# Performance work log

Hardware: AMD Instinct MI355X
Metric: run time of the kernel (lower is better)

## Reference

```python
import jax, jax.numpy as jnp
import numpy as np

WIN_SIZE = 16
STRIDE = 8
H = W = 512
B = 8
C = 3


def gaussian_blend(win_size):
    # matches WindowOverlapProcessor._create_gaussian_weights
    sigma = win_size / 4.0
    x = jnp.arange(win_size, dtype=jnp.float32) - (win_size - 1) / 2.0
    g = jnp.exp(-(x ** 2) / (2.0 * sigma ** 2))
    g = g / g.sum()
    return g[:, None] * g[None, :]  # [ws, ws]


def setup_inputs() -> dict:
    key = jax.random.key(0)
    hw = (H - WIN_SIZE) // STRIDE + 1  # 63
    ww = (W - WIN_SIZE) // STRIDE + 1  # 63
    nw = hw * ww  # 3969
    hs = (jnp.arange(hw) * STRIDE).astype(jnp.int64 if jax.config.jax_enable_x64 else jnp.int32)
    ws_ = (jnp.arange(ww) * STRIDE).astype(hs.dtype)
    coords = jnp.stack(
        [jnp.repeat(hs, ww), jnp.tile(ws_, hw)], axis=-1
    )  # [nw, 2] regular overlapping grid
    windows = jax.random.normal(key, (B, nw, WIN_SIZE, WIN_SIZE, C), dtype=jnp.float32)
    return {
        "windows": windows,
        "window_coords": coords,
        "h_windows": hw,
        "w_windows": ww,
        "stride": STRIDE,
        "original_h": H,
        "original_w": W,
        "channels": C,
    }


def reference(windows, window_coords, h_windows, w_windows, stride,
              original_h, original_w, channels):
    Bb, nw, ws, _, Cc = windows.shape
    blend = gaussian_blend(ws)  # [ws, ws]

    # flat pixel index for every window element
    dh = jnp.arange(ws)
    dw = jnp.arange(ws)
    offs = dh[:, None] * original_w + dw[None, :]            # [ws, ws]
    base = window_coords[:, 0] * original_w + window_coords[:, 1]  # [nw]
    idx = (base[:, None, None] + offs[None]).reshape(-1)     # [nw*ws*ws]

    # weighted window values, [B, C, nw*ws*ws]
    contrib = windows * blend[None, None, :, :, None]
    contrib = contrib.transpose(0, 4, 1, 2, 3).reshape(Bb, Cc, -1)

    recon = jnp.zeros((Bb, Cc, original_h * original_w), windows.dtype)
    recon = recon.at[:, :, idx].add(contrib)

    wsum = jnp.zeros((original_h * original_w,), blend.dtype)
    wsum = wsum.at[idx].add(jnp.tile(blend.reshape(-1), nw))

    recon = recon / (wsum[None, None, :] + 1e-8)
    return recon.reshape(Bb, Cc, original_h, original_w)
```

## Files before the change

kernel.cpp:

```cpp
#include <hip/hip_runtime.h>


#define OH 512
#define OW 512
#define NB 8
#define NC 3
#define HWIN 63
#define NWIN (HWIN * HWIN)
#define PLANE (OH * OW)
#define CH_F4 96
#define NCHUNK 34
#define NF4 (NCHUNK * CH_F4)
#define NSTRIPE (NF4 / 64)
#define STRIPE_PAD 65

typedef float f4 __attribute__((ext_vector_type(4)));
typedef unsigned int u32;

__device__ __forceinline__ float gblend(int d) {
    const float x = (float)d - 7.5f;
    return __expf(-(x * x) * 0.03125f) * 0.1044284f;
}

__device__ __forceinline__ int pof(int F) { return F + (F >> 6); }

__device__ __forceinline__ void async_ld16(const f4* gsrc, f4* ldst) {
    __builtin_amdgcn_global_load_lds(
        (const __attribute__((address_space(1))) u32*)gsrc,
        (__attribute__((address_space(3))) u32*)ldst, 16, 0, 0);
}

__global__ __launch_bounds__(256, 3) void window_overlap_kernel(
    const float* __restrict__ win, float* __restrict__ out) {
    __shared__ f4 lds[NSTRIPE * STRIPE_PAD];

    const int tid = threadIdx.x;
    const int bi = blockIdx.x;
    const int t = bi & 3;
    const int q = (bi >> 2) & 63;
    const int b = bi >> 8;

    const int qL = min(q, 62);
    const int qH = max(q - 1, 0);
    const int bOff = b * NWIN;

    const f4* __restrict__ w4 = (const f4*)win;
    const int wv = tid >> 6;
    const int lane = tid & 63;
    for (int s = wv; s < NSTRIPE; s += 4) {
        const int F = s * 64 + lane;
        const int c = F / 96;
        const int e = F - c * 96;
        const int hi = (c >= 17) ? 1 : 0;
        const int k = c - hi * 17;
        const int jj = min(max(16 * t - 1 + k, 0), HWIN - 1);
        const int qr = hi ? qH : qL;
        const int gidx = (bOff + qr * HWIN + jj) * 192 + hi * CH_F4 + e;
        async_ld16(w4 + gidx, &lds[s * STRIPE_PAD]);
    }
    __syncthreads();

    const int r = tid >> 5;
    const int w4p = (tid & 31) << 2;
    const int jl = w4p >> 3;
    const int c0 = w4p & 7;
    const int jg = 16 * t + jl;
    const float fB = (jg <= HWIN - 1) ? 1.0f : 0.0f;
    const float fA = (jg >= 1) ? 1.0f : 0.0f;
    const float wT = (q <= 62) ? gblend(r) : 0.0f;
    const float wB = (q >= 1) ? gblend(r + 8) : 0.0f;

    const int s0 = (c0 >> 2) * 3;
    const int rowf = r * 12;
    const int FLoB = (jl + 1) * 96 + rowf + s0;
    const int FLoA = jl * 96 + rowf + 6 + s0;
    const int FHiB = (18 + jl) * 96 + rowf + s0;
    const int FHiA = (17 + jl) * 96 + rowf + 6 + s0;

    f4 lb[3], la[3], hb[3], ha[3];
#pragma unroll
    for (int k = 0; k < 3; ++k) {
        lb[k] = lds[pof(FLoB + k)];
        la[k] = lds[pof(FLoA + k)];
        hb[k] = lds[pof(FHiB + k)];
        ha[k] = lds[pof(FHiA + k)];
    }

    const f4 gB = c0 ? (f4){0.0712141f, 0.0859006f, 0.0973380f, 0.1036157f}
                     : (f4){0.0180058f, 0.0278880f, 0.0405766f, 0.0554615f};
    const f4 gA = c0 ? (f4){0.0554615f, 0.0405766f, 0.0278880f, 0.0180058f}
                     : (f4){0.1036157f, 0.0973380f, 0.0859006f, 0.0712141f};

    f4 o[NC];
#pragma unroll
    for (int m = 0; m < 4; ++m) {
        const float wBc = fB * gB[m];
        const float wAc = fA * gA[m];
        const float rn = __builtin_amdgcn_rcpf((wT + wB) * (wAc + wBc) + 1e-8f);
#pragma unroll
        for (int ch = 0; ch < NC; ++ch) {
            const int f = 3 * m + ch;
            const float v = wT * (wAc * la[f >> 2][f & 3] + wBc * lb[f >> 2][f & 3]) +
                            wB * (wAc * ha[f >> 2][f & 3] + wBc * hb[f >> 2][f & 3]);
            o[ch][m] = v * rn;
        }
    }

    const int p = b * (NC * PLANE) + (8 * q + r) * OW + 128 * t + w4p;
    __builtin_nontemporal_store(o[0], (f4*)&out[p]);
    __builtin_nontemporal_store(o[1], (f4*)&out[p + PLANE]);
    __builtin_nontemporal_store(o[2], (f4*)&out[p + 2 * PLANE]);
}

extern "C" void kernel_launch(void* const* d_in, const int* in_sizes, int n_in,
                              void* d_out, int out_size, void* d_ws, size_t ws_size,
                              hipStream_t stream) {
    const float* windows = (const float*)d_in[0];
    float* out = (float*)d_out;
    window_overlap_kernel<<<2048, 256, 0, stream>>>(windows, out);
}
```

Before: 159.5 us.

## Split each tile into single-wave blocks covering two output rows

Each 256-thread block handling eight output rows is replaced by four 64-thread blocks, each handling two rows. A block now loads only the window rows it needs (24 float4 per chunk, padded to 25) into a smaller LDS buffer. The padding function is dropped and block indices are swizzled. The aim is higher occupancy and less LDS per block, so memory latency is better hidden and tail effects shrink. In exchange there are four times as many blocks, and nearby window data is fetched by separate blocks with more scattered loads.

New measurement: 159.8 us. No clear change (+0.2%).

```diff
diff --git a/kernel.cpp b/kernel.cpp
--- a/kernel.cpp
+++ b/kernel.cpp
@@ -8,11 +8,6 @@
 #define HWIN 63
 #define NWIN (HWIN * HWIN)
 #define PLANE (OH * OW)
-#define CH_F4 96
-#define NCHUNK 34
-#define NF4 (NCHUNK * CH_F4)
-#define NSTRIPE (NF4 / 64)
-#define STRIPE_PAD 65
 
 typedef float f4 __attribute__((ext_vector_type(4)));
 typedef unsigned int u32;
@@ -22,68 +17,71 @@
     return __expf(-(x * x) * 0.03125f) * 0.1044284f;
 }
 
-__device__ __forceinline__ int pof(int F) { return F + (F >> 6); }
-
 __device__ __forceinline__ void async_ld16(const f4* gsrc, f4* ldst) {
     __builtin_amdgcn_global_load_lds(
         (const __attribute__((address_space(1))) u32*)gsrc,
         (__attribute__((address_space(3))) u32*)ldst, 16, 0, 0);
 }
 
-__global__ __launch_bounds__(256, 3) void window_overlap_kernel(
+__global__ __launch_bounds__(64) void window_overlap_kernel(
     const float* __restrict__ win, float* __restrict__ out) {
-    __shared__ f4 lds[NSTRIPE * STRIPE_PAD];
+    __shared__ f4 lds[896];
 
-    const int tid = threadIdx.x;
     const int bi = blockIdx.x;
-    const int t = bi & 3;
-    const int q = (bi >> 2) & 63;
-    const int b = bi >> 8;
+    const int rp = (bi >> 3) & 3;
+    const int u = (bi & 7) | ((bi >> 5) << 3);
+    const int t = u & 3;
+    const int q = (u >> 2) & 63;
+    const int b = u >> 8;
+    const int r0 = rp << 1;
 
     const int qL = min(q, 62);
     const int qH = max(q - 1, 0);
     const int bOff = b * NWIN;
+    const int lane = threadIdx.x;
 
     const f4* __restrict__ w4 = (const f4*)win;
-    const int wv = tid >> 6;
-    const int lane = tid & 63;
-    for (int s = wv; s < NSTRIPE; s += 4) {
-        const int F = s * 64 + lane;
-        const int c = F / 96;
-        const int e = F - c * 96;
-        const int hi = (c >= 17) ? 1 : 0;
-        const int k = c - hi * 17;
-        const int jj = min(max(16 * t - 1 + k, 0), HWIN - 1);
+#pragma unroll
+    for (int i = 0; i < 14; ++i) {
+        const int P = i * 64 + lane;
+        int k = P / 25;
+        int e = P - k * 25;
+        k = min(k, 33);
+        e = min(e, 23);
+        const int hi = (k >= 17) ? 1 : 0;
+        const int kk = k - hi * 17;
+        const int jj = min(max(16 * t - 1 + kk, 0), HWIN - 1);
         const int qr = hi ? qH : qL;
-        const int gidx = (bOff + qr * HWIN + jj) * 192 + hi * CH_F4 + e;
-        async_ld16(w4 + gidx, &lds[s * STRIPE_PAD]);
+        const int gidx = (bOff + qr * HWIN + jj) * 192 + hi * 96 + r0 * 12 + e;
+        async_ld16(w4 + gidx, &lds[i * 64]);
     }
     __syncthreads();
 
-    const int r = tid >> 5;
-    const int w4p = (tid & 31) << 2;
+    const int rl = lane >> 5;
+    const int w4p = (lane & 31) << 2;
     const int jl = w4p >> 3;
     const int c0 = w4p & 7;
     const int jg = 16 * t + jl;
     const float fB = (jg <= HWIN - 1) ? 1.0f : 0.0f;
     const float fA = (jg >= 1) ? 1.0f : 0.0f;
+    const int r = r0 + rl;
     const float wT = (q <= 62) ? gblend(r) : 0.0f;
     const float wB = (q >= 1) ? gblend(r + 8) : 0.0f;
 
     const int s0 = (c0 >> 2) * 3;
-    const int rowf = r * 12;
-    const int FLoB = (jl + 1) * 96 + rowf + s0;
-    const int FLoA = jl * 96 + rowf + 6 + s0;
-    const int FHiB = (18 + jl) * 96 + rowf + s0;
-    const int FHiA = (17 + jl) * 96 + rowf + 6 + s0;
+    const int ro = rl * 12;
+    const int FLoB = (jl + 1) * 25 + ro + s0;
+    const int FLoA = jl * 25 + ro + 6 + s0;
+    const int FHiB = (18 + jl) * 25 + ro + s0;
+    const int FHiA = (17 + jl) * 25 + ro + 6 + s0;
 
     f4 lb[3], la[3], hb[3], ha[3];
 #pragma unroll
     for (int k = 0; k < 3; ++k) {
-        lb[k] = lds[pof(FLoB + k)];
-        la[k] = lds[pof(FLoA + k)];
-        hb[k] = lds[pof(FHiB + k)];
-        ha[k] = lds[pof(FHiA + k)];
+        lb[k] = lds[FLoB + k];
+        la[k] = lds[FLoA + k];
+        hb[k] = lds[FHiB + k];
+        ha[k] = lds[FHiA + k];
     }
 
     const f4 gB = c0 ? (f4){0.0712141f, 0.0859006f, 0.0973380f, 0.1036157f}
@@ -117,5 +115,5 @@
                               hipStream_t stream) {
     const float* windows = (const float*)d_in[0];
     float* out = (float*)d_out;
-    window_overlap_kernel<<<2048, 256, 0, stream>>>(windows, out);
+    window_overlap_kernel<<<8192, 64, 0, stream>>>(windows, out);
 }
```
